# Optimization experiments

Measured on AMD Instinct MI355X. Metric: run time of the kernel, lower is better.

The kernel has to match this reference:

```python
import jax, jax.numpy as jnp
import numpy as np

B, S, D = 4, 512, 256
VOCAB, MAX_RULES = 50257, 1024
EPS = 1e-12  # F.normalize default eps


def setup_inputs() -> dict:
    key = jax.random.key(0)
    k1, k2, k3, k4 = jax.random.split(key, 4)
    hidden_states = jax.random.normal(k1, (B, S, D), dtype=jnp.float32)
    token_ids = jax.random.randint(k2, (B, S), 0, VOCAB, dtype=jnp.int64)
    rule_transform = jax.random.normal(k3, (MAX_RULES, D, D), dtype=jnp.float32)
    token_rules = jax.random.randint(k4, (VOCAB,), 0, MAX_RULES, dtype=jnp.int64)
    return {
        "hidden_states": hidden_states,
        "token_ids": token_ids,
        "rule_transform": rule_transform,
        "token_rules": token_rules,
    }


def reference(hidden_states, token_ids, rule_transform, token_rules):
    # per-token rule index: [B, S]
    rule_indices = token_rules[token_ids]
    # gather DxD rule matrix per token: [B, S, D, D]
    rule_matrices = rule_transform[rule_indices]
    # F.normalize(p=2, dim=(-2,-1)): divide by Frobenius norm per matrix
    fro = jnp.sqrt(jnp.sum(rule_matrices * rule_matrices, axis=(-2, -1), keepdims=True))
    rule_matrices = rule_matrices / jnp.maximum(fro, EPS)
    # batched matvec: [B,S,D] x [B,S,D,E] -> [B,S,E]
    return jnp.einsum("bsd,bsde->bse", hidden_states, rule_matrices)
```

## Files before the change

### kernel.cpp

```cpp
#include <hip/hip_runtime.h>
#include <math.h>

#define D 256
#define NRULES 1024
#define TPB 8
#define NTOK_MAX 4096

__global__ __launch_bounds__(1024) void prep_kernel(
    const int* __restrict__ token_ids,
    const int* __restrict__ token_rules,
    int ntok,
    int* __restrict__ starts,
    int* __restrict__ bucket,
    int* __restrict__ worklist,
    int* __restrict__ nwork)
{
    __shared__ int cnt[NRULES];
    __shared__ int rtok[NTOK_MAX];
    __shared__ int wl[NRULES];
    __shared__ int wsum[16];
    __shared__ int nw;

    const int t    = threadIdx.x;
    const int wid  = t >> 6;
    const int lane = t & 63;

    cnt[t] = 0;
    if (t == 0) nw = 0;
    __syncthreads();

    for (int i = t; i < ntok; i += 1024) {
        const int r = token_rules[token_ids[i]];
        rtok[i] = r;
        atomicAdd(&cnt[r], 1);
    }
    __syncthreads();

    const int c = cnt[t];

    int v = c;
    #pragma unroll
    for (int off = 1; off < 64; off <<= 1) {
        const int u = __shfl_up(v, off, 64);
        if (lane >= off) v += u;
    }
    if (lane == 63) wsum[wid] = v;
    __syncthreads();
    if (t < 16) {
        const int w = wsum[t];
        int s = w;
        #pragma unroll
        for (int off = 1; off < 16; off <<= 1) {
            const int u = __shfl_up(s, off, 16);
            if (t >= off) s += u;
        }
        wsum[t] = s - w;
    }
    __syncthreads();

    const int excl = v - c + wsum[wid];
    starts[t] = excl;
    if (t == NRULES - 1) starts[NRULES] = excl + c;
    cnt[t] = excl;

    if (c > TPB) wl[atomicAdd(&nw, 1)] = t;
    __syncthreads();
    if (c > 0 && c <= TPB) wl[atomicAdd(&nw, 1)] = t;
    __syncthreads();

    for (int i = t; i < ntok; i += 1024) {
        const int pos = atomicAdd(&cnt[rtok[i]], 1);
        bucket[pos] = i;
    }

    const int nwv = nw;
    for (int i = t; i < nwv; i += 1024) worklist[i] = wl[i];
    if (t == 0) nwork[0] = nwv;
}

__global__ __launch_bounds__(256) void process_kernel(
    const float* __restrict__ hidden,
    const float* __restrict__ rules,
    const int*   __restrict__ starts,
    const int*   __restrict__ bucket,
    const int*   __restrict__ worklist,
    const int*   __restrict__ nwork,
    float* __restrict__ out)
{
    if ((int)blockIdx.x >= nwork[0]) return;
    const int r     = worklist[blockIdx.x];
    const int start = starts[r];
    const int count = starts[r + 1] - start;

    const int t    = threadIdx.x;
    const int wave = t >> 6;
    const int lane = t & 63;
    const int rr   = lane >> 4;
    const int col  = (wave << 6) + ((lane & 15) << 2);

    __shared__ float h_lds[TPB][D];
    __shared__ float sq_lds[4];
    __shared__ int   toks[TPB];

    const float* __restrict__ M = rules + (size_t)r * D * D;

    for (int base = 0; base < count; base += TPB) {
        if (t < TPB)
            toks[t] = (base + t < count) ? bucket[start + base + t] : -1;
        #pragma unroll
        for (int j = 0; j < TPB; ++j) {
            const int idx = base + j;
            h_lds[j][t] = (idx < count)
                ? hidden[(size_t)bucket[start + idx] * D + t] : 0.f;
        }
        __syncthreads();

        float4 acc[TPB];
        #pragma unroll
        for (int j = 0; j < TPB; ++j) acc[j] = float4{0.f, 0.f, 0.f, 0.f};
        float sq = 0.f;

        #pragma unroll 8
        for (int i = 0; i < 64; ++i) {
            const int d = (i << 2) + rr;
            const float4 m = *reinterpret_cast<const float4*>(M + (size_t)d * D + col);
            sq = fmaf(m.x, m.x, fmaf(m.y, m.y, fmaf(m.z, m.z, fmaf(m.w, m.w, sq))));
            #pragma unroll
            for (int j = 0; j < TPB; ++j) {
                const float h = h_lds[j][d];
                acc[j].x = fmaf(h, m.x, acc[j].x);
                acc[j].y = fmaf(h, m.y, acc[j].y);
                acc[j].z = fmaf(h, m.z, acc[j].z);
                acc[j].w = fmaf(h, m.w, acc[j].w);
            }
        }

        #pragma unroll
        for (int off = 32; off > 0; off >>= 1)
            sq += __shfl_down(sq, off, 64);
        if (lane == 0) sq_lds[wave] = sq;

        #pragma unroll
        for (int j = 0; j < TPB; ++j) {
            #pragma unroll
            for (int mask = 16; mask < 64; mask <<= 1) {
                acc[j].x += __shfl_xor(acc[j].x, mask, 64);
                acc[j].y += __shfl_xor(acc[j].y, mask, 64);
                acc[j].z += __shfl_xor(acc[j].z, mask, 64);
                acc[j].w += __shfl_xor(acc[j].w, mask, 64);
            }
        }
        __syncthreads();

        const float fro2 = sq_lds[0] + sq_lds[1] + sq_lds[2] + sq_lds[3];
        const float inv  = 1.0f / fmaxf(sqrtf(fro2), 1e-12f);

        #pragma unroll
        for (int j = 0; j < TPB; ++j) {
            if (rr == (j & 3)) {
                const int tok = toks[j];
                if (tok >= 0) {
                    float4 o;
                    o.x = acc[j].x * inv; o.y = acc[j].y * inv;
                    o.z = acc[j].z * inv; o.w = acc[j].w * inv;
                    *reinterpret_cast<float4*>(out + (size_t)tok * D + col) = o;
                }
            }
        }
        __syncthreads();
    }
}

extern "C" void kernel_launch(void* const* d_in, const int* in_sizes, int n_in,
                              void* d_out, int out_size, void* d_ws, size_t ws_size,
                              hipStream_t stream) {
    const float* hidden      = (const float*)d_in[0];
    const int*   token_ids   = (const int*)d_in[1];
    const float* rules       = (const float*)d_in[2];
    const int*   token_rules = (const int*)d_in[3];
    float*       out         = (float*)d_out;

    const int ntok = in_sizes[1];

    int* ws       = (int*)d_ws;
    int* starts   = ws;
    int* bucket   = starts + NRULES + 8;
    int* worklist = bucket + ntok;
    int* nwork    = worklist + NRULES;

    prep_kernel<<<1, 1024, 0, stream>>>(
        token_ids, token_rules, ntok, starts, bucket, worklist, nwork);
    process_kernel<<<NRULES, 256, 0, stream>>>(
        hidden, rules, starts, bucket, worklist, nwork, out);
}
```

Baseline: 51.11 us.

## Replace serial prefix-sum bucketing with parallel atomic fixed-slot buckets and spill list

Measured after the change: 50.74 us. No clear change (-0.7%).

```diff
diff --git a/kernel.cpp b/kernel.cpp
--- a/kernel.cpp
+++ b/kernel.cpp
@@ -4,114 +4,38 @@
 #define D 256
 #define NRULES 1024
 #define TPB 8
-#define NTOK_MAX 4096
+#define KMAX 16
 
-__global__ __launch_bounds__(1024) void prep_kernel(
-    const int* __restrict__ token_ids,
-    const int* __restrict__ token_rules,
-    int ntok,
-    int* __restrict__ starts,
-    int* __restrict__ bucket,
-    int* __restrict__ worklist,
-    int* __restrict__ nwork)
-{
-    __shared__ int cnt[NRULES];
-    __shared__ int rtok[NTOK_MAX];
-    __shared__ int wl[NRULES];
-    __shared__ int wsum[16];
-    __shared__ int nw;
-
-    const int t    = threadIdx.x;
-    const int wid  = t >> 6;
-    const int lane = t & 63;
-
-    cnt[t] = 0;
-    if (t == 0) nw = 0;
-    __syncthreads();
-
-    for (int i = t; i < ntok; i += 1024) {
-        const int r = token_rules[token_ids[i]];
-        rtok[i] = r;
-        atomicAdd(&cnt[r], 1);
-    }
-    __syncthreads();
-
-    const int c = cnt[t];
-
-    int v = c;
-    #pragma unroll
-    for (int off = 1; off < 64; off <<= 1) {
-        const int u = __shfl_up(v, off, 64);
-        if (lane >= off) v += u;
-    }
-    if (lane == 63) wsum[wid] = v;
-    __syncthreads();
-    if (t < 16) {
-        const int w = wsum[t];
-        int s = w;
-        #pragma unroll
-        for (int off = 1; off < 16; off <<= 1) {
-            const int u = __shfl_up(s, off, 16);
-            if (t >= off) s += u;
-        }
-        wsum[t] = s - w;
-    }
-    __syncthreads();
-
-    const int excl = v - c + wsum[wid];
-    starts[t] = excl;
-    if (t == NRULES - 1) starts[NRULES] = excl + c;
-    cnt[t] = excl;
-
-    if (c > TPB) wl[atomicAdd(&nw, 1)] = t;
-    __syncthreads();
-    if (c > 0 && c <= TPB) wl[atomicAdd(&nw, 1)] = t;
-    __syncthreads();
-
-    for (int i = t; i < ntok; i += 1024) {
-        const int pos = atomicAdd(&cnt[rtok[i]], 1);
-        bucket[pos] = i;
-    }
-
-    const int nwv = nw;
-    for (int i = t; i < nwv; i += 1024) worklist[i] = wl[i];
-    if (t == 0) nwork[0] = nwv;
+__global__ void prep_kernel(const int* __restrict__ token_ids,
+                            const int* __restrict__ token_rules,
+                            int ntok,
+                            int* __restrict__ counts,
+                            int* __restrict__ bucket,
+                            int* __restrict__ spill,
+                            int* __restrict__ nspill) {
+    const int i = blockIdx.x * blockDim.x + threadIdx.x;
+    if (i >= ntok) return;
+    const int r = token_rules[token_ids[i]];
+    const int slot = atomicAdd(&counts[r], 1);
+    if (slot < KMAX) bucket[r * KMAX + slot] = i;
+    else             spill[atomicAdd(nspill, 1)] = (r << 16) | i;
 }
 
-__global__ __launch_bounds__(256) void process_kernel(
+__device__ __forceinline__ void apply_rule(
+    const float* __restrict__ M,
+    const int* toks,
+    int count,
     const float* __restrict__ hidden,
-    const float* __restrict__ rules,
-    const int*   __restrict__ starts,
-    const int*   __restrict__ bucket,
-    const int*   __restrict__ worklist,
-    const int*   __restrict__ nwork,
-    float* __restrict__ out)
+    float* __restrict__ out,
+    float (*h_lds)[D], float* sq_lds,
+    int t, int wave, int lane, int rr, int col)
 {
-    if ((int)blockIdx.x >= nwork[0]) return;
-    const int r     = worklist[blockIdx.x];
-    const int start = starts[r];
-    const int count = starts[r + 1] - start;
-
-    const int t    = threadIdx.x;
-    const int wave = t >> 6;
-    const int lane = t & 63;
-    const int rr   = lane >> 4;
-    const int col  = (wave << 6) + ((lane & 15) << 2);
-
-    __shared__ float h_lds[TPB][D];
-    __shared__ float sq_lds[4];
-    __shared__ int   toks[TPB];
-
-    const float* __restrict__ M = rules + (size_t)r * D * D;
-
     for (int base = 0; base < count; base += TPB) {
-        if (t < TPB)
-            toks[t] = (base + t < count) ? bucket[start + base + t] : -1;
         #pragma unroll
         for (int j = 0; j < TPB; ++j) {
             const int idx = base + j;
             h_lds[j][t] = (idx < count)
-                ? hidden[(size_t)bucket[start + idx] * D + t] : 0.f;
+                ? hidden[(size_t)toks[idx] * D + t] : 0.f;
         }
         __syncthreads();
 
@@ -157,17 +81,54 @@
 
         #pragma unroll
         for (int j = 0; j < TPB; ++j) {
-            if (rr == (j & 3)) {
-                const int tok = toks[j];
-                if (tok >= 0) {
-                    float4 o;
-                    o.x = acc[j].x * inv; o.y = acc[j].y * inv;
-                    o.z = acc[j].z * inv; o.w = acc[j].w * inv;
-                    *reinterpret_cast<float4*>(out + (size_t)tok * D + col) = o;
-                }
+            if (rr == (j & 3) && base + j < count) {
+                const int tok = toks[base + j];
+                float4 o;
+                o.x = acc[j].x * inv; o.y = acc[j].y * inv;
+                o.z = acc[j].z * inv; o.w = acc[j].w * inv;
+                *reinterpret_cast<float4*>(out + (size_t)tok * D + col) = o;
             }
         }
         __syncthreads();
+    }
+}
+
+__global__ __launch_bounds__(256) void process_kernel(
+    const float* __restrict__ hidden,
+    const float* __restrict__ rules,
+    const int*   __restrict__ counts,
+    const int*   __restrict__ bucket,
+    const int*   __restrict__ spill,
+    const int*   __restrict__ nspill,
+    float* __restrict__ out)
+{
+    const int b    = blockIdx.x;
+    const int t    = threadIdx.x;
+    const int wave = t >> 6;
+    const int lane = t & 63;
+    const int rr   = lane >> 4;
+    const int col  = (wave << 6) + ((lane & 15) << 2);
+
+    __shared__ float h_lds[TPB][D];
+    __shared__ float sq_lds[4];
+    __shared__ int   toks[KMAX];
+
+    const int cnt = min(counts[b], KMAX);
+    if (cnt > 0) {
+        if (t < cnt) toks[t] = bucket[b * KMAX + t];
+        __syncthreads();
+        apply_rule(rules + (size_t)b * D * D, toks, cnt,
+                   hidden, out, h_lds, sq_lds, t, wave, lane, rr, col);
+    }
+
+    const int ns = nspill[0];
+    for (int k = b; k < ns; k += gridDim.x) {
+        __syncthreads();
+        const int e = spill[k];
+        if (t == 0) toks[0] = e & 0xFFFF;
+        __syncthreads();
+        apply_rule(rules + (size_t)(e >> 16) * D * D, toks, 1,
+                   hidden, out, h_lds, sq_lds, t, wave, lane, rr, col);
     }
 }
 
@@ -182,14 +143,15 @@
 
     const int ntok = in_sizes[1];
 
-    int* ws       = (int*)d_ws;
-    int* starts   = ws;
-    int* bucket   = starts + NRULES + 8;
-    int* worklist = bucket + ntok;
-    int* nwork    = worklist + NRULES;
+    int* ws     = (int*)d_ws;
+    int* counts = ws;
+    int* nspill = ws + NRULES;
+    int* bucket = ws + NRULES + 8;
+    int* spill  = bucket + NRULES * KMAX;
 
-    prep_kernel<<<1, 1024, 0, stream>>>(
-        token_ids, token_rules, ntok, starts, bucket, worklist, nwork);
+    hipMemsetAsync(counts, 0, (NRULES + 8) * sizeof(int), stream);
+    prep_kernel<<<(ntok + 255) / 256, 256, 0, stream>>>(
+        token_ids, token_rules, ntok, counts, bucket, spill, nspill);
     process_kernel<<<NRULES, 256, 0, stream>>>(
-        hidden, rules, starts, bucket, worklist, nwork, out);
+        hidden, rules, counts, bucket, spill, nspill, out);
 }
```
